# Kernel optimization log

Hardware: AMD Instinct MI355X
Metric: run time of the kernel (lower is better)

Reference implementation:

```python
import jax, jax.numpy as jnp
import numpy as np

DIM = 128; NH = 4; WH = 7; WW = 7
B = 16; H = 112; W = 112
SH, SW = WH // 2, WW // 2          # shift sizes (3,3)
NWIN = WH * WW                     # 49 tokens per window
HEAD = DIM // NH


def _rel_pos_index():
    ch, cw = np.meshgrid(np.arange(WH), np.arange(WW), indexing='ij')
    coords = np.stack([ch, cw]).reshape(2, -1)            # (2, NWIN)
    rel = coords[:, :, None] - coords[:, None, :]          # (2, NWIN, NWIN)
    rel = rel.transpose(1, 2, 0).copy()
    rel[:, :, 0] += WH - 1
    rel[:, :, 1] += WW - 1
    rel[:, :, 0] *= 2 * WW - 1
    return rel.sum(-1)                                     # (NWIN, NWIN) int


def _shift_mask():
    img = np.zeros((H, W), dtype=np.float32)
    cnt = 0
    for hs in (slice(0, -WH), slice(-WH, -SH), slice(-SH, None)):
        for ws in (slice(0, -WW), slice(-WW, -SW), slice(-SW, None)):
            img[hs, ws] = cnt
            cnt += 1
    mw = img.reshape(H // WH, WH, W // WW, WW).transpose(0, 2, 1, 3).reshape(-1, NWIN)
    diff = mw[:, None, :] - mw[:, :, None]                 # (nW, NWIN, NWIN)
    return np.where(diff != 0, -100.0, 0.0).astype(np.float32)


REL_IDX = jnp.asarray(_rel_pos_index())                    # (NWIN, NWIN) int32
MASK = jnp.asarray(_shift_mask())                          # (nW, NWIN, NWIN)


def setup_inputs() -> dict:
    key = jax.random.key(0)
    k = jax.random.split(key, 6)
    s = 0.02
    return {
        'x': jax.random.normal(k[0], (B, H, W, DIM), dtype=jnp.float32),
        'qkv_w': jax.random.normal(k[1], (3 * DIM, DIM), dtype=jnp.float32) * s,
        'qkv_b': jnp.zeros((3 * DIM,), dtype=jnp.float32),
        'proj_w': jax.random.normal(k[2], (DIM, DIM), dtype=jnp.float32) * s,
        'proj_b': jnp.zeros((DIM,), dtype=jnp.float32),
        'rpb_table': jax.random.normal(k[3], ((2 * WH - 1) * (2 * WW - 1), NH), dtype=jnp.float32) * s,
    }


def reference(x, qkv_w, qkv_b, proj_w, proj_b, rpb_table):
    scale = HEAD ** -0.5
    Bx, Hh, Ww, C = x.shape
    Nh, Nw = Hh // WH, Ww // WW
    nW = Nh * Nw
    # cyclic shift
    x = jnp.roll(x, shift=(-SH, -SW), axis=(1, 2))
    # window partition -> (B*nW, NWIN, C)
    xw = x.reshape(Bx, Nh, WH, Nw, WW, C).transpose(0, 1, 3, 2, 4, 5).reshape(-1, NWIN, C)
    # fused qkv projection, split (T, Nh, P) on last dim
    qkv = (xw @ qkv_w.T + qkv_b).reshape(-1, NWIN, 3, NH, HEAD).transpose(2, 0, 3, 1, 4)
    q, k, v = qkv[0] * scale, qkv[1], qkv[2]               # (Bn, NH, NWIN, HEAD)
    attn = jnp.einsum('bhid,bhjd->bhij', q, k)             # (Bn, NH, NWIN, NWIN)
    # relative position bias gather
    bias = rpb_table[REL_IDX.reshape(-1)].reshape(NWIN, NWIN, NH).transpose(2, 0, 1)
    attn = attn + bias[None]
    # shift mask (broadcast over batch and heads)
    attn = attn.reshape(Bx, nW, NH, NWIN, NWIN) + MASK[None, :, None]
    attn = jax.nn.softmax(attn, axis=-1).reshape(-1, NH, NWIN, NWIN)
    out = jnp.einsum('bhij,bhjd->bhid', attn, v)           # (Bn, NH, NWIN, HEAD)
    out = out.transpose(0, 2, 1, 3).reshape(-1, NWIN, C)   # head-major concat
    out = out @ proj_w.T + proj_b
    # window merge + reverse shift
    out = out.reshape(Bx, Nh, Nw, WH, WW, C).transpose(0, 1, 3, 2, 4, 5).reshape(Bx, Hh, Ww, C)
    out = jnp.roll(out, shift=(SH, SW), axis=(1, 2))
    return out
```

## Files before the change

### kernel.cpp

```cpp
#include <hip/hip_runtime.h>
#include <hip/hip_bf16.h>

typedef __attribute__((ext_vector_type(8))) short short8;
typedef __attribute__((ext_vector_type(4))) float floatx4;

#define IMGH 112
#define IMGW 112
#define SHIFT 3
#define NWIN 49

#define XSTR 152
#define QKSTR 280
#define VTSTR 88

#define LOG2E 1.4426950408889634f
#define QSCALE (0.17677669529663687f * LOG2E)
#define NMASK (-100.0f * LOG2E)

__device__ inline unsigned short f2bf1(float f) {
    unsigned r;
    asm("v_cvt_pk_bf16_f32 %0, %1, %1" : "=v"(r) : "v"(f));
    return (unsigned short)r;
}
__device__ inline unsigned cvtpk(float lo, float hi) {
    unsigned r;
    asm("v_cvt_pk_bf16_f32 %0, %1, %2" : "=v"(r) : "v"(lo), "v"(hi));
    return r;
}

__device__ inline floatx4 mfma16(short8 a, short8 b, floatx4 c) {
    return __builtin_amdgcn_mfma_f32_16x16x32_bf16(a, b, c, 0, 0, 0);
}
__device__ inline floatx4 zero4() {
    floatx4 z; z[0] = 0.f; z[1] = 0.f; z[2] = 0.f; z[3] = 0.f; return z;
}
__device__ inline short8 ones8() {
    short8 z;
    #pragma unroll
    for (int i = 0; i < 8; ++i) z[i] = (short)0x3F80;
    return z;
}

__global__ __launch_bounds__(256) void convert_w(const float* __restrict__ qkv_w,
                                                 const float* __restrict__ proj_w,
                                                 short* __restrict__ ws) {
    int i = blockIdx.x * 256 + threadIdx.x;
    if (i < 49152) {
        float v = qkv_w[i];
        if (i < 16384) v *= QSCALE;
        ws[i] = (short)f2bf1(v);
    }
    if (i < 16384) ws[49152 + i] = (short)f2bf1(proj_w[i]);
}

__global__ __launch_bounds__(512, 4) void win_attn_mfma8(
    const float* __restrict__ x,
    const float* __restrict__ qkv_b,
    const float* __restrict__ proj_b,
    const float* __restrict__ rpb,
    const short* __restrict__ wq,
    const short* __restrict__ wp,
    float* __restrict__ out)
{
    __shared__ alignas(16) short s_xp[64 * XSTR];
    __shared__ alignas(16) short s_qk[64 * QKSTR];
    __shared__ alignas(16) short s_vt[128 * VTSTR];
    __shared__ float2 s_rpb[2][169];
    __shared__ int s_meta[64];
    __shared__ int s_gout[64];

    const int tid = threadIdx.x;
    const int w    = tid >> 6;
    const int l    = tid & 63;
    const int l15  = l & 15;
    const int lg   = l >> 4;
    const int hgrp = w >> 2;
    const int m_w  = w & 3;
    const int swz  = (l15 & 3) << 4;

    const int blk = blockIdx.x;
    const int b   = blk >> 8;
    const int wi  = blk & 255;
    const int hs0 = (wi >> 4) * 7;
    const int ws0 = (wi & 15) * 7;

    const float* xb = x + (size_t)b * (IMGH * IMGW * 128);

    if (tid < 64) {
        int rowc = tid < NWIN ? tid : NWIN - 1;
        int ri = (rowc * 9363) >> 16;
        int ci = rowc - ri * 7;
        int hc = hs0 + ri, wc = ws0 + ci;
        int reg = (hc < 105 ? 0 : (hc < 109 ? 1 : 2)) * 3
                + (wc < 105 ? 0 : (wc < 109 ? 1 : 2));
        if (tid >= NWIN) reg = 255;
        s_meta[tid] = (ri * 13 + ci) | (reg << 8);
        int gh = hc + SHIFT; if (gh >= IMGH) gh -= IMGH;
        int gw = wc + SHIFT; if (gw >= IMGW) gw -= IMGW;
        s_gout[tid] = gh * IMGW + gw;
    }
    if (tid < 338) {
        int hg  = tid < 169 ? 0 : 1;
        int idx = tid - hg * 169;
        float2 v = *(const float2*)(rpb + idx * 4 + hg * 2);
        v.x *= LOG2E; v.y *= LOG2E;
        s_rpb[hg][idx] = v;
    }
    {
        int row  = tid >> 3;
        int col0 = (tid & 7) << 4;
        int cs   = col0 ^ ((row & 3) << 4);
        uint4 u0 = {0,0,0,0}, u1 = {0,0,0,0};
        if (row < NWIN) {
            int rr = (row * 9363) >> 16;
            int cc = row - rr * 7;
            int gh = hs0 + rr + SHIFT; if (gh >= IMGH) gh -= IMGH;
            int gw = ws0 + cc + SHIFT; if (gw >= IMGW) gw -= IMGW;
            const float* px = xb + (((size_t)(gh * IMGW + gw)) << 7) + col0;
            float4 a = *(const float4*)(px + 0);
            float4 c4 = *(const float4*)(px + 4);
            float4 e = *(const float4*)(px + 8);
            float4 g = *(const float4*)(px + 12);
            u0.x = cvtpk(a.x, a.y);   u0.y = cvtpk(a.z, a.w);
            u0.z = cvtpk(c4.x, c4.y); u0.w = cvtpk(c4.z, c4.w);
            u1.x = cvtpk(e.x, e.y);   u1.y = cvtpk(e.z, e.w);
            u1.z = cvtpk(g.x, g.y);   u1.w = cvtpk(g.z, g.w);
        }
        *(uint4*)&s_xp[row * XSTR + cs]     = u0;
        *(uint4*)&s_xp[row * XSTR + cs + 8] = u1;
    }
    __syncthreads();

    {
        short8 bfr[3][4];
        float4 biasq[3];
        float  biasv[3];
        #pragma unroll
        for (int i = 0; i < 3; ++i) {
            int j0 = (w * 3 + i) << 4;
            const short* wb = wq + ((j0 + l15) << 7) + lg * 8;
            #pragma unroll
            for (int kk = 0; kk < 4; ++kk) bfr[i][kk] = *(const short8*)(wb + kk * 32);
            float4 b4 = *(const float4*)(qkv_b + j0 + lg * 4);
            if (j0 < 128) { b4.x *= QSCALE; b4.y *= QSCALE; b4.z *= QSCALE; b4.w *= QSCALE; }
            biasq[i] = b4;
            biasv[i] = qkv_b[j0 + l15];
        }
        for (int m = 0; m < 4; ++m) {
            short8 af[4];
            #pragma unroll
            for (int kk = 0; kk < 4; ++kk)
                af[kk] = *(const short8*)&s_xp[(m * 16 + l15) * XSTR + ((kk * 32 + lg * 8) ^ swz)];
            #pragma unroll
            for (int i = 0; i < 3; ++i) {
                int j0 = (w * 3 + i) << 4;
                if (j0 < 256) {
                    floatx4 acc = zero4();
                    #pragma unroll
                    for (int kk = 0; kk < 4; ++kk) acc = mfma16(bfr[i][kk], af[kk], acc);
                    uint2 u;
                    u.x = cvtpk(acc[0] + biasq[i].x, acc[1] + biasq[i].y);
                    u.y = cvtpk(acc[2] + biasq[i].z, acc[3] + biasq[i].w);
                    *(uint2*)&s_qk[(m * 16 + l15) * QKSTR + ((j0 + lg * 4) ^ swz)] = u;
                } else {
                    floatx4 acc = zero4();
                    #pragma unroll
                    for (int kk = 0; kk < 4; ++kk) acc = mfma16(af[kk], bfr[i][kk], acc);
                    uint2 u;
                    u.x = cvtpk(acc[0] + biasv[i], acc[1] + biasv[i]);
                    u.y = cvtpk(acc[2] + biasv[i], acc[3] + biasv[i]);
                    *(uint2*)&s_vt[(j0 - 256 + l15) * VTSTR + ((m * 16 + lg * 4) ^ swz)] = u;
                }
            }
        }
    }
    __syncthreads();

    float b2x[4][4], b2y[4][4];
    {
        int mi = s_meta[m_w * 16 + l15];
        int ti = mi & 255, gi = mi >> 8;
        #pragma unroll
        for (int n = 0; n < 4; ++n) {
            int4 mk = *(const int4*)&s_meta[n * 16 + lg * 4];
            #pragma unroll
            for (int c = 0; c < 4; ++c) {
                int mv = (&mk.x)[c];
                int d = ti - (mv & 255) + 84;
                float msk = (gi == (mv >> 8)) ? 0.f : NMASK;
                float2 r2 = s_rpb[hgrp][d];
                b2x[n][c] = r2.x + msk;
                b2y[n][c] = r2.y + msk;
            }
        }
    }

    floatx4 accO[2][2];
    float   inv2[2];
    const short8 vone = ones8();
    #pragma unroll
    for (int hh = 0; hh < 2; ++hh) {
        const int h = hgrp * 2 + hh;
        short8 qf = *(const short8*)&s_qk[(m_w * 16 + l15) * QKSTR + ((h * 32 + lg * 8) ^ swz)];
        floatx4 accS[4];
        #pragma unroll
        for (int n = 0; n < 4; ++n) {
            short8 kf = *(const short8*)&s_qk[(n * 16 + l15) * QKSTR + (128 + ((h * 32 + lg * 8) ^ swz))];
            accS[n] = mfma16(kf, qf, zero4());
        }
        #pragma unroll
        for (int n = 0; n < 4; ++n) {
            float p0 = exp2f(accS[n][0] + (hh ? b2y[n][0] : b2x[n][0]));
            float p1 = exp2f(accS[n][1] + (hh ? b2y[n][1] : b2x[n][1]));
            float p2 = exp2f(accS[n][2] + (hh ? b2y[n][2] : b2x[n][2]));
            float p3 = exp2f(accS[n][3] + (hh ? b2y[n][3] : b2x[n][3]));
            uint2 u;
            u.x = cvtpk(p0, p1);
            u.y = cvtpk(p2, p3);
            *(uint2*)&s_xp[(m_w * 16 + l15) * XSTR + hgrp * 72 + ((n * 16 + lg * 4) ^ swz)] = u;
        }
        short8 pa[2];
        #pragma unroll
        for (int kt = 0; kt < 2; ++kt)
            pa[kt] = *(const short8*)&s_xp[(m_w * 16 + l15) * XSTR + hgrp * 72 + ((kt * 32 + lg * 8) ^ swz)];
        floatx4 accSum = zero4();
        #pragma unroll
        for (int vt = 0; vt < 2; ++vt) accO[hh][vt] = zero4();
        #pragma unroll
        for (int kt = 0; kt < 2; ++kt) {
            #pragma unroll
            for (int vt = 0; vt < 2; ++vt) {
                short8 vf = *(const short8*)&s_vt[(h * 32 + vt * 16 + l15) * VTSTR + ((kt * 32 + lg * 8) ^ swz)];
                accO[hh][vt] = mfma16(vf, pa[kt], accO[hh][vt]);
            }
            accSum = mfma16(vone, pa[kt], accSum);
        }
        inv2[hh] = 1.f / accSum[0];
    }
    __syncthreads();

    #pragma unroll
    for (int hh = 0; hh < 2; ++hh)
        #pragma unroll
        for (int vt = 0; vt < 2; ++vt) {
            uint2 u;
            u.x = cvtpk(accO[hh][vt][0] * inv2[hh], accO[hh][vt][1] * inv2[hh]);
            u.y = cvtpk(accO[hh][vt][2] * inv2[hh], accO[hh][vt][3] * inv2[hh]);
            *(uint2*)&s_xp[(m_w * 16 + l15) * XSTR + hgrp * 64 + ((hh * 32 + vt * 16 + lg * 4) ^ swz)] = u;
        }
    __syncthreads();

    {
        floatx4 acc[4];
        #pragma unroll
        for (int m = 0; m < 4; ++m) acc[m] = zero4();
        const short* wbp = wp + ((w * 16 + l15) << 7) + lg * 8;
        #pragma unroll
        for (int kk = 0; kk < 4; ++kk) {
            short8 pw = *(const short8*)(wbp + kk * 32);
            #pragma unroll
            for (int m = 0; m < 4; ++m) {
                short8 of = *(const short8*)&s_xp[(m * 16 + l15) * XSTR + ((kk * 32 + lg * 8) ^ swz)];
                acc[m] = mfma16(pw, of, acc[m]);
            }
        }
        float4 pb = *(const float4*)(proj_b + w * 16 + lg * 4);
        const size_t obase = (size_t)b * (IMGH * IMGW);
        #pragma unroll
        for (int m = 0; m < 4; ++m) {
            int token = m * 16 + l15;
            if (token < NWIN) {
                float4 o4;
                o4.x = acc[m][0] + pb.x;
                o4.y = acc[m][1] + pb.y;
                o4.z = acc[m][2] + pb.z;
                o4.w = acc[m][3] + pb.w;
                *(float4*)&out[((obase + s_gout[token]) << 7) + w * 16 + lg * 4] = o4;
            }
        }
    }
}

extern "C" void kernel_launch(void* const* d_in, const int* in_sizes, int n_in,
                              void* d_out, int out_size, void* d_ws, size_t ws_size,
                              hipStream_t stream) {
    const float* x      = (const float*)d_in[0];
    const float* qkv_w  = (const float*)d_in[1];
    const float* qkv_b  = (const float*)d_in[2];
    const float* proj_w = (const float*)d_in[3];
    const float* proj_b = (const float*)d_in[4];
    const float* rpb    = (const float*)d_in[5];
    float* out = (float*)d_out;
    short* wbf = (short*)d_ws;

    hipLaunchKernelGGL(convert_w, dim3(192), dim3(256), 0, stream, qkv_w, proj_w, wbf);
    hipLaunchKernelGGL(win_attn_mfma8, dim3(4096), dim3(512), 0, stream,
                       x, qkv_b, proj_b, rpb, wbf, wbf + 49152, out);
}
```

Before: 115.1 us.

## Split window attention across 16 waves with one head per wave

```diff
diff --git a/kernel.cpp b/kernel.cpp
--- a/kernel.cpp
+++ b/kernel.cpp
@@ -53,7 +53,7 @@
     if (i < 16384) ws[49152 + i] = (short)f2bf1(proj_w[i]);
 }
 
-__global__ __launch_bounds__(512, 4) void win_attn_mfma8(
+__global__ __launch_bounds__(1024, 8) void win_attn_mfma16(
     const float* __restrict__ x,
     const float* __restrict__ qkv_b,
     const float* __restrict__ proj_b,
@@ -74,8 +74,8 @@
     const int l    = tid & 63;
     const int l15  = l & 15;
     const int lg   = l >> 4;
-    const int hgrp = w >> 2;
-    const int m_w  = w & 3;
+    const int h2   = w >> 2;
+    const int mq   = w & 3;
     const int swz  = (l15 & 3) << 4;
 
     const int blk = blockIdx.x;
@@ -107,10 +107,10 @@
         s_rpb[hg][idx] = v;
     }
     {
-        int row  = tid >> 3;
-        int col0 = (tid & 7) << 4;
+        int row  = tid >> 4;
+        int col0 = (tid & 15) << 3;
         int cs   = col0 ^ ((row & 3) << 4);
-        uint4 u0 = {0,0,0,0}, u1 = {0,0,0,0};
+        uint2 u0 = {0, 0}, u1 = {0, 0};
         if (row < NWIN) {
             int rr = (row * 9363) >> 16;
             int cc = row - rr * 7;
@@ -119,56 +119,49 @@
             const float* px = xb + (((size_t)(gh * IMGW + gw)) << 7) + col0;
             float4 a = *(const float4*)(px + 0);
             float4 c4 = *(const float4*)(px + 4);
-            float4 e = *(const float4*)(px + 8);
-            float4 g = *(const float4*)(px + 12);
             u0.x = cvtpk(a.x, a.y);   u0.y = cvtpk(a.z, a.w);
-            u0.z = cvtpk(c4.x, c4.y); u0.w = cvtpk(c4.z, c4.w);
-            u1.x = cvtpk(e.x, e.y);   u1.y = cvtpk(e.z, e.w);
-            u1.z = cvtpk(g.x, g.y);   u1.w = cvtpk(g.z, g.w);
-        }
-        *(uint4*)&s_xp[row * XSTR + cs]     = u0;
-        *(uint4*)&s_xp[row * XSTR + cs + 8] = u1;
-    }
-    __syncthreads();
-
-    {
-        short8 bfr[3][4];
-        float4 biasq[3];
-        float  biasv[3];
-        #pragma unroll
-        for (int i = 0; i < 3; ++i) {
-            int j0 = (w * 3 + i) << 4;
-            const short* wb = wq + ((j0 + l15) << 7) + lg * 8;
-            #pragma unroll
-            for (int kk = 0; kk < 4; ++kk) bfr[i][kk] = *(const short8*)(wb + kk * 32);
-            float4 b4 = *(const float4*)(qkv_b + j0 + lg * 4);
-            if (j0 < 128) { b4.x *= QSCALE; b4.y *= QSCALE; b4.z *= QSCALE; b4.w *= QSCALE; }
-            biasq[i] = b4;
-            biasv[i] = qkv_b[j0 + l15];
-        }
-        for (int m = 0; m < 4; ++m) {
+            u1.x = cvtpk(c4.x, c4.y); u1.y = cvtpk(c4.z, c4.w);
+        }
+        *(uint2*)&s_xp[row * XSTR + cs]     = u0;
+        *(uint2*)&s_xp[row * XSTR + cs + 4] = u1;
+    }
+    __syncthreads();
+
+    {
+        const int mh = w >> 3;
+        #pragma unroll
+        for (int m2 = 0; m2 < 2; ++m2) {
+            const int m = mh * 2 + m2;
             short8 af[4];
             #pragma unroll
             for (int kk = 0; kk < 4; ++kk)
                 af[kk] = *(const short8*)&s_xp[(m * 16 + l15) * XSTR + ((kk * 32 + lg * 8) ^ swz)];
             #pragma unroll
             for (int i = 0; i < 3; ++i) {
-                int j0 = (w * 3 + i) << 4;
+                const int n  = 3 * (w & 7) + i;
+                const int j0 = n << 4;
+                const short* wb = wq + ((j0 + l15) << 7) + lg * 8;
+                short8 bfr[4];
+                #pragma unroll
+                for (int kk = 0; kk < 4; ++kk) bfr[kk] = *(const short8*)(wb + kk * 32);
                 if (j0 < 256) {
+                    float4 b4 = *(const float4*)(qkv_b + j0 + lg * 4);
+                    if (j0 < 128) { b4.x *= QSCALE; b4.y *= QSCALE; b4.z *= QSCALE; b4.w *= QSCALE; }
                     floatx4 acc = zero4();
                     #pragma unroll
-                    for (int kk = 0; kk < 4; ++kk) acc = mfma16(bfr[i][kk], af[kk], acc);
+                    for (int kk = 0; kk < 4; ++kk) acc = mfma16(bfr[kk], af[kk], acc);
                     uint2 u;
-                    u.x = cvtpk(acc[0] + biasq[i].x, acc[1] + biasq[i].y);
-                    u.y = cvtpk(acc[2] + biasq[i].z, acc[3] + biasq[i].w);
+                    u.x = cvtpk(acc[0] + b4.x, acc[1] + b4.y);
+                    u.y = cvtpk(acc[2] + b4.z, acc[3] + b4.w);
                     *(uint2*)&s_qk[(m * 16 + l15) * QKSTR + ((j0 + lg * 4) ^ swz)] = u;
                 } else {
+                    float bv = qkv_b[j0 + l15];
                     floatx4 acc = zero4();
                     #pragma unroll
-                    for (int kk = 0; kk < 4; ++kk) acc = mfma16(af[kk], bfr[i][kk], acc);
+                    for (int kk = 0; kk < 4; ++kk) acc = mfma16(af[kk], bfr[kk], acc);
                     uint2 u;
-                    u.x = cvtpk(acc[0] + biasv[i], acc[1] + biasv[i]);
-                    u.y = cvtpk(acc[2] + biasv[i], acc[3] + biasv[i]);
+                    u.x = cvtpk(acc[0] + bv, acc[1] + bv);
+                    u.y = cvtpk(acc[2] + bv, acc[3] + bv);
                     *(uint2*)&s_vt[(j0 - 256 + l15) * VTSTR + ((m * 16 + lg * 4) ^ swz)] = u;
                 }
             }
@@ -176,9 +169,16 @@
     }
     __syncthreads();
 
-    float b2x[4][4], b2y[4][4];
-    {
-        int mi = s_meta[m_w * 16 + l15];
+    short8 qf = *(const short8*)&s_qk[(mq * 16 + l15) * QKSTR + ((h2 * 32 + lg * 8) ^ swz)];
+    floatx4 accS[4];
+    #pragma unroll
+    for (int n = 0; n < 4; ++n) {
+        short8 kf = *(const short8*)&s_qk[(n * 16 + l15) * QKSTR + ((128 + h2 * 32 + lg * 8) ^ swz)];
+        accS[n] = mfma16(kf, qf, zero4());
+    }
+    float bh[4][4];
+    {
+        int mi = s_meta[mq * 16 + l15];
         int ti = mi & 255, gi = mi >> 8;
         #pragma unroll
         for (int n = 0; n < 4; ++n) {
@@ -188,94 +188,80 @@
                 int mv = (&mk.x)[c];
                 int d = ti - (mv & 255) + 84;
                 float msk = (gi == (mv >> 8)) ? 0.f : NMASK;
-                float2 r2 = s_rpb[hgrp][d];
-                b2x[n][c] = r2.x + msk;
-                b2y[n][c] = r2.y + msk;
-            }
-        }
-    }
-
-    floatx4 accO[2][2];
-    float   inv2[2];
-    const short8 vone = ones8();
+                float2 r2 = s_rpb[h2 >> 1][d];
+                bh[n][c] = ((h2 & 1) ? r2.y : r2.x) + msk;
+            }
+        }
+    }
+    __syncthreads();
+
     #pragma unroll
-    for (int hh = 0; hh < 2; ++hh) {
-        const int h = hgrp * 2 + hh;
-        short8 qf = *(const short8*)&s_qk[(m_w * 16 + l15) * QKSTR + ((h * 32 + lg * 8) ^ swz)];
-        floatx4 accS[4];
-        #pragma unroll
-        for (int n = 0; n < 4; ++n) {
-            short8 kf = *(const short8*)&s_qk[(n * 16 + l15) * QKSTR + (128 + ((h * 32 + lg * 8) ^ swz))];
-            accS[n] = mfma16(kf, qf, zero4());
-        }
-        #pragma unroll
-        for (int n = 0; n < 4; ++n) {
-            float p0 = exp2f(accS[n][0] + (hh ? b2y[n][0] : b2x[n][0]));
-            float p1 = exp2f(accS[n][1] + (hh ? b2y[n][1] : b2x[n][1]));
-            float p2 = exp2f(accS[n][2] + (hh ? b2y[n][2] : b2x[n][2]));
-            float p3 = exp2f(accS[n][3] + (hh ? b2y[n][3] : b2x[n][3]));
-            uint2 u;
-            u.x = cvtpk(p0, p1);
-            u.y = cvtpk(p2, p3);
-            *(uint2*)&s_xp[(m_w * 16 + l15) * XSTR + hgrp * 72 + ((n * 16 + lg * 4) ^ swz)] = u;
-        }
+    for (int n = 0; n < 4; ++n) {
+        float p0 = exp2f(accS[n][0] + bh[n][0]);
+        float p1 = exp2f(accS[n][1] + bh[n][1]);
+        float p2 = exp2f(accS[n][2] + bh[n][2]);
+        float p3 = exp2f(accS[n][3] + bh[n][3]);
+        uint2 u;
+        u.x = cvtpk(p0, p1);
+        u.y = cvtpk(p2, p3);
+        *(uint2*)&s_qk[(mq * 16 + l15) * QKSTR + ((h2 * 64 + n * 16 + lg * 4) ^ swz)] = u;
+    }
+    {
+        const short8 vone = ones8();
         short8 pa[2];
         #pragma unroll
         for (int kt = 0; kt < 2; ++kt)
-            pa[kt] = *(const short8*)&s_xp[(m_w * 16 + l15) * XSTR + hgrp * 72 + ((kt * 32 + lg * 8) ^ swz)];
-        floatx4 accSum = zero4();
-        #pragma unroll
-        for (int vt = 0; vt < 2; ++vt) accO[hh][vt] = zero4();
+            pa[kt] = *(const short8*)&s_qk[(mq * 16 + l15) * QKSTR + ((h2 * 64 + kt * 32 + lg * 8) ^ swz)];
+        floatx4 accO[2], accSum = zero4();
+        #pragma unroll
+        for (int vt = 0; vt < 2; ++vt) accO[vt] = zero4();
         #pragma unroll
         for (int kt = 0; kt < 2; ++kt) {
             #pragma unroll
             for (int vt = 0; vt < 2; ++vt) {
-                short8 vf = *(const short8*)&s_vt[(h * 32 + vt * 16 + l15) * VTSTR + ((kt * 32 + lg * 8) ^ swz)];
-                accO[hh][vt] = mfma16(vf, pa[kt], accO[hh][vt]);
+                short8 vf = *(const short8*)&s_vt[(h2 * 32 + vt * 16 + l15) * VTSTR + ((kt * 32 + lg * 8) ^ swz)];
+                accO[vt] = mfma16(vf, pa[kt], accO[vt]);
             }
             accSum = mfma16(vone, pa[kt], accSum);
         }
-        inv2[hh] = 1.f / accSum[0];
-    }
-    __syncthreads();
-
-    #pragma unroll
-    for (int hh = 0; hh < 2; ++hh)
+        float inv = 1.f / accSum[0];
         #pragma unroll
         for (int vt = 0; vt < 2; ++vt) {
             uint2 u;
-            u.x = cvtpk(accO[hh][vt][0] * inv2[hh], accO[hh][vt][1] * inv2[hh]);
-            u.y = cvtpk(accO[hh][vt][2] * inv2[hh], accO[hh][vt][3] * inv2[hh]);
-            *(uint2*)&s_xp[(m_w * 16 + l15) * XSTR + hgrp * 64 + ((hh * 32 + vt * 16 + lg * 4) ^ swz)] = u;
-        }
-    __syncthreads();
-
-    {
-        floatx4 acc[4];
-        #pragma unroll
-        for (int m = 0; m < 4; ++m) acc[m] = zero4();
-        const short* wbp = wp + ((w * 16 + l15) << 7) + lg * 8;
-        #pragma unroll
-        for (int kk = 0; kk < 4; ++kk) {
-            short8 pw = *(const short8*)(wbp + kk * 32);
-            #pragma unroll
-            for (int m = 0; m < 4; ++m) {
-                short8 of = *(const short8*)&s_xp[(m * 16 + l15) * XSTR + ((kk * 32 + lg * 8) ^ swz)];
-                acc[m] = mfma16(pw, of, acc[m]);
-            }
-        }
-        float4 pb = *(const float4*)(proj_b + w * 16 + lg * 4);
+            u.x = cvtpk(accO[vt][0] * inv, accO[vt][1] * inv);
+            u.y = cvtpk(accO[vt][2] * inv, accO[vt][3] * inv);
+            *(uint2*)&s_xp[(mq * 16 + l15) * XSTR + ((h2 * 32 + vt * 16 + lg * 4) ^ swz)] = u;
+        }
+    }
+    __syncthreads();
+
+    {
+        const int n3 = w & 7, mh3 = w >> 3;
+        const int j0 = n3 << 4;
+        const short* wbp = wp + ((j0 + l15) << 7) + lg * 8;
+        short8 pw[4];
+        #pragma unroll
+        for (int kk = 0; kk < 4; ++kk) pw[kk] = *(const short8*)(wbp + kk * 32);
+        float4 pb = *(const float4*)(proj_b + j0 + lg * 4);
         const size_t obase = (size_t)b * (IMGH * IMGW);
         #pragma unroll
-        for (int m = 0; m < 4; ++m) {
+        for (int m2 = 0; m2 < 2; ++m2) {
+            const int m = mh3 * 2 + m2;
+            short8 of[4];
+            #pragma unroll
+            for (int kk = 0; kk < 4; ++kk)
+                of[kk] = *(const short8*)&s_xp[(m * 16 + l15) * XSTR + ((kk * 32 + lg * 8) ^ swz)];
+            floatx4 acc = zero4();
+            #pragma unroll
+            for (int kk = 0; kk < 4; ++kk) acc = mfma16(pw[kk], of[kk], acc);
             int token = m * 16 + l15;
             if (token < NWIN) {
                 float4 o4;
-                o4.x = acc[m][0] + pb.x;
-                o4.y = acc[m][1] + pb.y;
-                o4.z = acc[m][2] + pb.z;
-                o4.w = acc[m][3] + pb.w;
-                *(float4*)&out[((obase + s_gout[token]) << 7) + w * 16 + lg * 4] = o4;
+                o4.x = acc[0] + pb.x;
+                o4.y = acc[1] + pb.y;
+                o4.z = acc[2] + pb.z;
+                o4.w = acc[3] + pb.w;
+                *(float4*)&out[((obase + s_gout[token]) << 7) + j0 + lg * 4] = o4;
             }
         }
     }
@@ -294,6 +280,6 @@
     short* wbf = (short*)d_ws;
 
     hipLaunchKernelGGL(convert_w, dim3(192), dim3(256), 0, stream, qkv_w, proj_w, wbf);
-    hipLaunchKernelGGL(win_attn_mfma8, dim3(4096), dim3(512), 0, stream,
+    hipLaunchKernelGGL(win_attn_mfma16, dim3(4096), dim3(1024), 0, stream,
                        x, qkv_b, proj_b, rpb, wbf, wbf + 49152, out);
 }
```

Measured after the change: 381.7 us. +231.6%, slower.

## Shrink LDS footprint and registers to raise occupancy to six blocks per CU

Applied to the files above, without the earlier changes.

```diff
diff --git a/kernel.cpp b/kernel.cpp
--- a/kernel.cpp
+++ b/kernel.cpp
@@ -9,9 +9,9 @@
 #define SHIFT 3
 #define NWIN 49
 
-#define XSTR 152
-#define QKSTR 280
-#define VTSTR 88
+#define XSTR 144
+#define QKSTR 264
+#define VTSTR 72
 
 #define LOG2E 1.4426950408889634f
 #define QSCALE (0.17677669529663687f * LOG2E)
@@ -26,6 +26,9 @@
     unsigned r;
     asm("v_cvt_pk_bf16_f32 %0, %1, %2" : "=v"(r) : "v"(lo), "v"(hi));
     return r;
+}
+__device__ inline float bf2f(short s) {
+    return __uint_as_float(((unsigned)(unsigned short)s) << 16);
 }
 
 __device__ inline floatx4 mfma16(short8 a, short8 b, floatx4 c) {
@@ -53,7 +56,7 @@
     if (i < 16384) ws[49152 + i] = (short)f2bf1(proj_w[i]);
 }
 
-__global__ __launch_bounds__(512, 4) void win_attn_mfma8(
+__global__ __launch_bounds__(512, 6) void win_attn_mfma8d(
     const float* __restrict__ x,
     const float* __restrict__ qkv_b,
     const float* __restrict__ proj_b,
@@ -62,12 +65,13 @@
     const short* __restrict__ wp,
     float* __restrict__ out)
 {
-    __shared__ alignas(16) short s_xp[64 * XSTR];
+    __shared__ alignas(16) short s_a [64 * XSTR];
     __shared__ alignas(16) short s_qk[64 * QKSTR];
-    __shared__ alignas(16) short s_vt[128 * VTSTR];
-    __shared__ float2 s_rpb[2][169];
+    __shared__ short s_rpbh[4 * 170];
     __shared__ int s_meta[64];
     __shared__ int s_gout[64];
+
+    short* s_vt = s_a;
 
     const int tid = threadIdx.x;
     const int w    = tid >> 6;
@@ -99,12 +103,8 @@
         int gw = wc + SHIFT; if (gw >= IMGW) gw -= IMGW;
         s_gout[tid] = gh * IMGW + gw;
     }
-    if (tid < 338) {
-        int hg  = tid < 169 ? 0 : 1;
-        int idx = tid - hg * 169;
-        float2 v = *(const float2*)(rpb + idx * 4 + hg * 2);
-        v.x *= LOG2E; v.y *= LOG2E;
-        s_rpb[hg][idx] = v;
+    for (int idx = tid; idx < 676; idx += 512) {
+        s_rpbh[(idx & 3) * 170 + (idx >> 2)] = (short)f2bf1(rpb[idx] * LOG2E);
     }
     {
         int row  = tid >> 3;
@@ -126,74 +126,78 @@
             u1.x = cvtpk(e.x, e.y);   u1.y = cvtpk(e.z, e.w);
             u1.z = cvtpk(g.x, g.y);   u1.w = cvtpk(g.z, g.w);
         }
-        *(uint4*)&s_xp[row * XSTR + cs]     = u0;
-        *(uint4*)&s_xp[row * XSTR + cs + 8] = u1;
-    }
-    __syncthreads();
-
+        *(uint4*)&s_a[row * XSTR + cs]     = u0;
+        *(uint4*)&s_a[row * XSTR + cs + 8] = u1;
+    }
+    __syncthreads();
+
+    uint2 vreg[4];
     {
-        short8 bfr[3][4];
-        float4 biasq[3];
-        float  biasv[3];
-        #pragma unroll
-        for (int i = 0; i < 3; ++i) {
-            int j0 = (w * 3 + i) << 4;
-            const short* wb = wq + ((j0 + l15) << 7) + lg * 8;
-            #pragma unroll
-            for (int kk = 0; kk < 4; ++kk) bfr[i][kk] = *(const short8*)(wb + kk * 32);
-            float4 b4 = *(const float4*)(qkv_b + j0 + lg * 4);
-            if (j0 < 128) { b4.x *= QSCALE; b4.y *= QSCALE; b4.z *= QSCALE; b4.w *= QSCALE; }
-            biasq[i] = b4;
-            biasv[i] = qkv_b[j0 + l15];
-        }
+        const int j0v = 256 + (w << 4);
+        const short* wbv = wq + ((j0v + l15) << 7) + lg * 8;
+        short8 bfrv[4];
+        #pragma unroll
+        for (int kk = 0; kk < 4; ++kk) bfrv[kk] = *(const short8*)(wbv + kk * 32);
+        const float bv = qkv_b[j0v + l15];
+
+        const int j00 = w << 5;
+        const short* wb0 = wq + ((j00 + l15) << 7) + lg * 8;
+        short8 bfr0[4];
+        #pragma unroll
+        for (int kk = 0; kk < 4; ++kk) bfr0[kk] = *(const short8*)(wb0 + kk * 32);
+        float4 b40 = *(const float4*)(qkv_b + j00 + lg * 4);
+        if (j00 < 128) { b40.x *= QSCALE; b40.y *= QSCALE; b40.z *= QSCALE; b40.w *= QSCALE; }
+
+        #pragma unroll
         for (int m = 0; m < 4; ++m) {
             short8 af[4];
             #pragma unroll
             for (int kk = 0; kk < 4; ++kk)
-                af[kk] = *(const short8*)&s_xp[(m * 16 + l15) * XSTR + ((kk * 32 + lg * 8) ^ swz)];
-            #pragma unroll
-            for (int i = 0; i < 3; ++i) {
-                int j0 = (w * 3 + i) << 4;
-                if (j0 < 256) {
-                    floatx4 acc = zero4();
-                    #pragma unroll
-                    for (int kk = 0; kk < 4; ++kk) acc = mfma16(bfr[i][kk], af[kk], acc);
-                    uint2 u;
-                    u.x = cvtpk(acc[0] + biasq[i].x, acc[1] + biasq[i].y);
-                    u.y = cvtpk(acc[2] + biasq[i].z, acc[3] + biasq[i].w);
-                    *(uint2*)&s_qk[(m * 16 + l15) * QKSTR + ((j0 + lg * 4) ^ swz)] = u;
-                } else {
-                    floatx4 acc = zero4();
-                    #pragma unroll
-                    for (int kk = 0; kk < 4; ++kk) acc = mfma16(af[kk], bfr[i][kk], acc);
-                    uint2 u;
-                    u.x = cvtpk(acc[0] + biasv[i], acc[1] + biasv[i]);
-                    u.y = cvtpk(acc[2] + biasv[i], acc[3] + biasv[i]);
-                    *(uint2*)&s_vt[(j0 - 256 + l15) * VTSTR + ((m * 16 + lg * 4) ^ swz)] = u;
-                }
-            }
-        }
-    }
-    __syncthreads();
-
-    float b2x[4][4], b2y[4][4];
-    {
-        int mi = s_meta[m_w * 16 + l15];
-        int ti = mi & 255, gi = mi >> 8;
-        #pragma unroll
-        for (int n = 0; n < 4; ++n) {
-            int4 mk = *(const int4*)&s_meta[n * 16 + lg * 4];
-            #pragma unroll
-            for (int c = 0; c < 4; ++c) {
-                int mv = (&mk.x)[c];
-                int d = ti - (mv & 255) + 84;
-                float msk = (gi == (mv >> 8)) ? 0.f : NMASK;
-                float2 r2 = s_rpb[hgrp][d];
-                b2x[n][c] = r2.x + msk;
-                b2y[n][c] = r2.y + msk;
-            }
-        }
-    }
+                af[kk] = *(const short8*)&s_a[(m * 16 + l15) * XSTR + ((kk * 32 + lg * 8) ^ swz)];
+            floatx4 av = zero4(), a0 = zero4();
+            #pragma unroll
+            for (int kk = 0; kk < 4; ++kk) {
+                av = mfma16(af[kk], bfrv[kk], av);
+                a0 = mfma16(bfr0[kk], af[kk], a0);
+            }
+            vreg[m].x = cvtpk(av[0] + bv, av[1] + bv);
+            vreg[m].y = cvtpk(av[2] + bv, av[3] + bv);
+            uint2 u;
+            u.x = cvtpk(a0[0] + b40.x, a0[1] + b40.y);
+            u.y = cvtpk(a0[2] + b40.z, a0[3] + b40.w);
+            *(uint2*)&s_qk[(m * 16 + l15) * QKSTR + ((j00 + lg * 4) ^ swz)] = u;
+        }
+
+        const int j01 = j00 + 16;
+        const short* wb1 = wq + ((j01 + l15) << 7) + lg * 8;
+        short8 bfr1[4];
+        #pragma unroll
+        for (int kk = 0; kk < 4; ++kk) bfr1[kk] = *(const short8*)(wb1 + kk * 32);
+        float4 b41 = *(const float4*)(qkv_b + j01 + lg * 4);
+        if (j01 < 128) { b41.x *= QSCALE; b41.y *= QSCALE; b41.z *= QSCALE; b41.w *= QSCALE; }
+        #pragma unroll
+        for (int m = 0; m < 4; ++m) {
+            short8 af[4];
+            #pragma unroll
+            for (int kk = 0; kk < 4; ++kk)
+                af[kk] = *(const short8*)&s_a[(m * 16 + l15) * XSTR + ((kk * 32 + lg * 8) ^ swz)];
+            floatx4 a1 = zero4();
+            #pragma unroll
+            for (int kk = 0; kk < 4; ++kk) a1 = mfma16(bfr1[kk], af[kk], a1);
+            uint2 u;
+            u.x = cvtpk(a1[0] + b41.x, a1[1] + b41.y);
+            u.y = cvtpk(a1[2] + b41.z, a1[3] + b41.w);
+            *(uint2*)&s_qk[(m * 16 + l15) * QKSTR + ((j01 + lg * 4) ^ swz)] = u;
+        }
+    }
+    __syncthreads();
+
+    #pragma unroll
+    for (int m = 0; m < 4; ++m)
+        *(uint2*)&s_vt[(w * 16 + l15) * VTSTR + ((m * 16 + lg * 4) ^ swz)] = vreg[m];
+    short8 qf0 = *(const short8*)&s_qk[(m_w * 16 + l15) * QKSTR + (((hgrp * 2 + 0) * 32 + lg * 8) ^ swz)];
+    short8 qf1 = *(const short8*)&s_qk[(m_w * 16 + l15) * QKSTR + (((hgrp * 2 + 1) * 32 + lg * 8) ^ swz)];
+    __syncthreads();
 
     floatx4 accO[2][2];
     float   inv2[2];
@@ -201,28 +205,38 @@
     #pragma unroll
     for (int hh = 0; hh < 2; ++hh) {
         const int h = hgrp * 2 + hh;
-        short8 qf = *(const short8*)&s_qk[(m_w * 16 + l15) * QKSTR + ((h * 32 + lg * 8) ^ swz)];
+        short8 qf = hh ? qf1 : qf0;
         floatx4 accS[4];
         #pragma unroll
         for (int n = 0; n < 4; ++n) {
             short8 kf = *(const short8*)&s_qk[(n * 16 + l15) * QKSTR + (128 + ((h * 32 + lg * 8) ^ swz))];
             accS[n] = mfma16(kf, qf, zero4());
         }
-        #pragma unroll
-        for (int n = 0; n < 4; ++n) {
-            float p0 = exp2f(accS[n][0] + (hh ? b2y[n][0] : b2x[n][0]));
-            float p1 = exp2f(accS[n][1] + (hh ? b2y[n][1] : b2x[n][1]));
-            float p2 = exp2f(accS[n][2] + (hh ? b2y[n][2] : b2x[n][2]));
-            float p3 = exp2f(accS[n][3] + (hh ? b2y[n][3] : b2x[n][3]));
-            uint2 u;
-            u.x = cvtpk(p0, p1);
-            u.y = cvtpk(p2, p3);
-            *(uint2*)&s_xp[(m_w * 16 + l15) * XSTR + hgrp * 72 + ((n * 16 + lg * 4) ^ swz)] = u;
+        {
+            int mi = s_meta[m_w * 16 + l15];
+            int ti = mi & 255, gi = mi >> 8;
+            const short* rh = s_rpbh + h * 170;
+            #pragma unroll
+            for (int n = 0; n < 4; ++n) {
+                int4 mk = *(const int4*)&s_meta[n * 16 + lg * 4];
+                float pv[4];
+                #pragma unroll
+                for (int c = 0; c < 4; ++c) {
+                    int mv = (&mk.x)[c];
+                    int d = ti - (mv & 255) + 84;
+                    float bias = bf2f(rh[d]) + ((gi == (mv >> 8)) ? 0.f : NMASK);
+                    pv[c] = exp2f(accS[n][c] + bias);
+                }
+                uint2 u;
+                u.x = cvtpk(pv[0], pv[1]);
+                u.y = cvtpk(pv[2], pv[3]);
+                *(uint2*)&s_qk[(m_w * 16 + l15) * QKSTR + hgrp * 64 + ((n * 16 + lg * 4) ^ swz)] = u;
+            }
         }
         short8 pa[2];
         #pragma unroll
         for (int kt = 0; kt < 2; ++kt)
-            pa[kt] = *(const short8*)&s_xp[(m_w * 16 + l15) * XSTR + hgrp * 72 + ((kt * 32 + lg * 8) ^ swz)];
+            pa[kt] = *(const short8*)&s_qk[(m_w * 16 + l15) * QKSTR + hgrp * 64 + ((kt * 32 + lg * 8) ^ swz)];
         floatx4 accSum = zero4();
         #pragma unroll
         for (int vt = 0; vt < 2; ++vt) accO[hh][vt] = zero4();
@@ -246,7 +260,7 @@
             uint2 u;
             u.x = cvtpk(accO[hh][vt][0] * inv2[hh], accO[hh][vt][1] * inv2[hh]);
             u.y = cvtpk(accO[hh][vt][2] * inv2[hh], accO[hh][vt][3] * inv2[hh]);
-            *(uint2*)&s_xp[(m_w * 16 + l15) * XSTR + hgrp * 64 + ((hh * 32 + vt * 16 + lg * 4) ^ swz)] = u;
+            *(uint2*)&s_a[(m_w * 16 + l15) * XSTR + ((hgrp * 64 + hh * 32 + vt * 16 + lg * 4) ^ swz)] = u;
         }
     __syncthreads();
 
@@ -260,7 +274,7 @@
             short8 pw = *(const short8*)(wbp + kk * 32);
             #pragma unroll
             for (int m = 0; m < 4; ++m) {
-                short8 of = *(const short8*)&s_xp[(m * 16 + l15) * XSTR + ((kk * 32 + lg * 8) ^ swz)];
+                short8 of = *(const short8*)&s_a[(m * 16 + l15) * XSTR + ((kk * 32 + lg * 8) ^ swz)];
                 acc[m] = mfma16(pw, of, acc[m]);
             }
         }
@@ -275,7 +289,7 @@
                 o4.y = acc[m][1] + pb.y;
                 o4.z = acc[m][2] + pb.z;
                 o4.w = acc[m][3] + pb.w;
-                *(float4*)&out[((obase + s_gout[token]) << 7) + w * 16 + lg * 4] = o4;
+                *(float4*)&out[((obase + s_gout[token]) << 7) + (w << 4) + lg * 4] = o4;
             }
         }
     }
@@ -294,6 +308,6 @@
     short* wbf = (short*)d_ws;
 
     hipLaunchKernelGGL(convert_w, dim3(192), dim3(256), 0, stream, qkv_w, proj_w, wbf);
-    hipLaunchKernelGGL(win_attn_mfma8, dim3(4096), dim3(512), 0, stream,
+    hipLaunchKernelGGL(win_attn_mfma8d, dim3(4096), dim3(512), 0, stream,
                        x, qkv_b, proj_b, rpb, wbf, wbf + 49152, out);
 }
```

Result: slower. 171.5 us (+49.0%).
